# Performance work log

Hardware: AMD Instinct MI355X
Metric: run time of the kernel (lower is better)

The kernel has to match this reference:

```python
import jax, jax.numpy as jnp
import numpy as np

B, R, S, P = 32768, 16, 128, 128  # particles, rotations, num_sphs, num_projections


def setup_inputs() -> dict:
    key = jax.random.key(0)
    k1, k2, k3 = jax.random.split(key, 3)
    weight_scale = np.sqrt(6.0 / (S + P))  # RandomUniform(-scale, scale) init
    x_real = jax.random.normal(k1, (B, R, S), dtype=jnp.float32)
    x_imag = jax.random.normal(k2, (B, R, S), dtype=jnp.float32)
    projection = jax.random.uniform(k3, (R, S, P), dtype=jnp.float32,
                                    minval=-weight_scale, maxval=weight_scale)
    return {"x_real": x_real, "x_imag": x_imag, "projection": projection}


def reference(x_real, x_imag, projection):
    # complex input (B, R, S); real weight (R, S, P) cast to complex64
    x = jax.lax.complex(x_real, x_imag)
    w = projection.astype(x.dtype)
    # contraction over num_sphs (fused GEMM instead of expand_dims*mul+sum)
    sph_projected = jnp.einsum('brs,rsp->brp', x, w)  # (B, R, P) complex64
    # conversion == 'abs'
    return jnp.abs(sph_projected)
```

## Files before the change

### kernel.cpp

```cpp
#include <hip/hip_runtime.h>
#include <hip/hip_bf16.h>
#include <math.h>


typedef __attribute__((ext_vector_type(8))) __bf16 bf16x8;
typedef __attribute__((ext_vector_type(4))) float f32x4;

#define R_TOT 16
#define S_TOT 128
#define P_TOT 128
#define RS 2048
#define RP 2048
#define ROWS_PER_BLOCK 256
#define STRIP 16
#define NSTRIPS (ROWS_PER_BLOCK / STRIP)

typedef const __attribute__((address_space(1))) void* gas_t;
typedef __attribute__((address_space(3))) void* las_t;

__global__ __launch_bounds__(256, 3) void cproj_kernel(
    const float* __restrict__ x_real,
    const float* __restrict__ x_imag,
    const float* __restrict__ proj,
    float* __restrict__ out)
{
    __shared__ __attribute__((aligned(16))) float xb[2][2][STRIP][128];

    const int tid  = threadIdx.x;
    const int r    = blockIdx.x & 15;
    const int br   = blockIdx.x >> 4;
    const int lane = tid & 63;
    const int wid  = tid >> 6;
    const int m    = lane & 15;
    const int g    = lane >> 4;
    const int b_base = br * ROWS_PER_BLOCK;

    const int st_arr = wid >> 1;
    const int st_r0  = (wid & 1) * 8;
    const float* xsrc = (st_arr == 0) ? x_real : x_imag;

#define STAGE(bufi, strip_)                                                    \
    do {                                                                       \
        _Pragma("unroll")                                                      \
        for (int i = 0; i < 4; ++i) {                                          \
            const int row = st_r0 + 2 * i + (lane >> 5);                       \
            const int gb  = b_base + (strip_) * STRIP + row;                   \
            const float* gp = xsrc + (size_t)gb * RS + r * S_TOT               \
                              + (((lane & 31) ^ (row & 7)) << 2);              \
            __builtin_amdgcn_global_load_lds(                                  \
                (gas_t)gp, (las_t)&xb[bufi][st_arr][st_r0 + 2 * i][0],         \
                16, 0, 0);                                                     \
        }                                                                      \
    } while (0)

    STAGE(0, 0);

    bf16x8 wf[2][4];
    {
        const float* wrp = proj + (size_t)r * (S_TOT * P_TOT) + wid * 32 + m;
        #pragma unroll
        for (int nt = 0; nt < 2; ++nt) {
            #pragma unroll
            for (int kk = 0; kk < 4; ++kk) {
                bf16x8 w;
                #pragma unroll
                for (int j = 0; j < 8; ++j) {
                    w[j] = (__bf16)wrp[(size_t)(kk * 32 + g * 8 + j) * P_TOT
                                       + nt * 16];
                }
                wf[nt][kk] = w;
            }
        }
    }
    __syncthreads();

    for (int s = 0; s < NSTRIPS; ++s) {
        const int buf = s & 1;
        if (s + 1 < NSTRIPS) STAGE(buf ^ 1, s + 1);
        __builtin_amdgcn_sched_barrier(0);

        bf16x8 ar[2][4];
        #pragma unroll
        for (int a = 0; a < 2; ++a) {
            #pragma unroll
            for (int kk = 0; kk < 4; ++kk) {
                const int c0 = kk * 8 + 2 * g;
                const int s0 = (c0 ^ (m & 7)) << 2;
                const int s1 = ((c0 + 1) ^ (m & 7)) << 2;
                f32x4 lo = *(const f32x4*)&xb[buf][a][m][s0];
                f32x4 hi = *(const f32x4*)&xb[buf][a][m][s1];
                bf16x8 t;
                #pragma unroll
                for (int j = 0; j < 4; ++j) {
                    t[j]     = (__bf16)lo[j];
                    t[j + 4] = (__bf16)hi[j];
                }
                ar[a][kk] = t;
            }
        }

        f32x4 acc[2][2];
        #pragma unroll
        for (int nt = 0; nt < 2; ++nt) {
            acc[nt][0] = (f32x4)0.0f;
            acc[nt][1] = (f32x4)0.0f;
        }
        #pragma unroll
        for (int kk = 0; kk < 4; ++kk) {
            #pragma unroll
            for (int nt = 0; nt < 2; ++nt) {
                acc[nt][0] = __builtin_amdgcn_mfma_f32_16x16x32_bf16(
                    ar[0][kk], wf[nt][kk], acc[nt][0], 0, 0, 0);
                acc[nt][1] = __builtin_amdgcn_mfma_f32_16x16x32_bf16(
                    ar[1][kk], wf[nt][kk], acc[nt][1], 0, 0, 0);
            }
        }

        float ov[2][4];
        #pragma unroll
        for (int nt = 0; nt < 2; ++nt) {
            #pragma unroll
            for (int j = 0; j < 4; ++j) {
                float re = acc[nt][0][j];
                float im = acc[nt][1][j];
                ov[nt][j] = sqrtf(re * re + im * im);
            }
        }

        if (s + 1 < NSTRIPS) __syncthreads();

        float* po = out + (size_t)(b_base + s * STRIP + g * 4) * RP
                    + r * P_TOT + wid * 32 + m;
        #pragma unroll
        for (int nt = 0; nt < 2; ++nt) {
            #pragma unroll
            for (int j = 0; j < 4; ++j) {
                po[(size_t)j * RP + nt * 16] = ov[nt][j];
            }
        }
    }
#undef STAGE
}

extern "C" void kernel_launch(void* const* d_in, const int* in_sizes, int n_in,
                              void* d_out, int out_size, void* d_ws, size_t ws_size,
                              hipStream_t stream) {
    const float* x_real = (const float*)d_in[0];
    const float* x_imag = (const float*)d_in[1];
    const float* proj   = (const float*)d_in[2];
    float* out = (float*)d_out;

    dim3 grid(R_TOT * 128);
    dim3 block(256);
    cproj_kernel<<<grid, block, 0, stream>>>(x_real, x_imag, proj, out);
}
```

Before: 155.8 us.

## Triple-buffer strip staging with explicit vmcnt waits and fully unrolled loop

Replaces the double-buffered LDS staging with a three-deep ring that prefetches two strips ahead. Each strip is guarded by an explicit s_waitcnt vmcnt count plus a raw s_barrier instead of __syncthreads, and the strip loop is unrolled by hand so those counts can be literal constants. The intent is to keep more global loads in flight and let output stores stay outstanding instead of draining at each barrier. This uses more LDS, which may cut occupancy, and correctness depends on the hand-counted vmcnt values matching the real numbers of loads and stores in flight.

```diff
diff --git a/kernel.cpp b/kernel.cpp
--- a/kernel.cpp
+++ b/kernel.cpp
@@ -13,7 +13,7 @@
 #define RP 2048
 #define ROWS_PER_BLOCK 256
 #define STRIP 16
-#define NSTRIPS (ROWS_PER_BLOCK / STRIP)
+#define NSTRIPS 16
 
 typedef const __attribute__((address_space(1))) void* gas_t;
 typedef __attribute__((address_space(3))) void* las_t;
@@ -24,7 +24,7 @@
     const float* __restrict__ proj,
     float* __restrict__ out)
 {
-    __shared__ __attribute__((aligned(16))) float xb[2][2][STRIP][128];
+    __shared__ __attribute__((aligned(16))) float xb[3][2][STRIP][128];
 
     const int tid  = threadIdx.x;
     const int r    = blockIdx.x & 15;
@@ -39,21 +39,20 @@
     const int st_r0  = (wid & 1) * 8;
     const float* xsrc = (st_arr == 0) ? x_real : x_imag;
 
-#define STAGE(bufi, strip_)                                                    \
-    do {                                                                       \
-        _Pragma("unroll")                                                      \
-        for (int i = 0; i < 4; ++i) {                                          \
-            const int row = st_r0 + 2 * i + (lane >> 5);                       \
-            const int gb  = b_base + (strip_) * STRIP + row;                   \
-            const float* gp = xsrc + (size_t)gb * RS + r * S_TOT               \
-                              + (((lane & 31) ^ (row & 7)) << 2);              \
-            __builtin_amdgcn_global_load_lds(                                  \
-                (gas_t)gp, (las_t)&xb[bufi][st_arr][st_r0 + 2 * i][0],         \
-                16, 0, 0);                                                     \
-        }                                                                      \
+#define STAGE(strip_)                                                         \
+    do {                                                                      \
+        _Pragma("unroll")                                                     \
+        for (int i = 0; i < 4; ++i) {                                         \
+            const int row = st_r0 + 2 * i + (lane >> 5);                      \
+            const int gb  = b_base + (strip_) * STRIP + row;                  \
+            const float* gp = xsrc + (size_t)gb * RS + r * S_TOT              \
+                              + (((lane & 31) ^ (row & 7)) << 2);             \
+            __builtin_amdgcn_global_load_lds(                                 \
+                (gas_t)gp,                                                    \
+                (las_t)&xb[(strip_) % 3][st_arr][st_r0 + 2 * i][0],           \
+                16, 0, 0);                                                    \
+        }                                                                     \
     } while (0)
-
-    STAGE(0, 0);
 
     bf16x8 wf[2][4];
     {
@@ -72,73 +71,79 @@
             }
         }
     }
-    __syncthreads();
+    asm volatile("s_waitcnt vmcnt(0)" ::: "memory");
 
-    for (int s = 0; s < NSTRIPS; ++s) {
-        const int buf = s & 1;
-        if (s + 1 < NSTRIPS) STAGE(buf ^ 1, s + 1);
-        __builtin_amdgcn_sched_barrier(0);
+    STAGE(0);
+    STAGE(1);
 
-        bf16x8 ar[2][4];
-        #pragma unroll
-        for (int a = 0; a < 2; ++a) {
-            #pragma unroll
-            for (int kk = 0; kk < 4; ++kk) {
-                const int c0 = kk * 8 + 2 * g;
-                const int s0 = (c0 ^ (m & 7)) << 2;
-                const int s1 = ((c0 + 1) ^ (m & 7)) << 2;
-                f32x4 lo = *(const f32x4*)&xb[buf][a][m][s0];
-                f32x4 hi = *(const f32x4*)&xb[buf][a][m][s1];
-                bf16x8 t;
-                #pragma unroll
-                for (int j = 0; j < 4; ++j) {
-                    t[j]     = (__bf16)lo[j];
-                    t[j + 4] = (__bf16)hi[j];
-                }
-                ar[a][kk] = t;
-            }
-        }
+#define ITER(s_, vm_)                                                         \
+    {                                                                         \
+        asm volatile("s_waitcnt vmcnt(" #vm_ ")" ::: "memory");               \
+        __builtin_amdgcn_s_barrier();                                         \
+        __builtin_amdgcn_sched_barrier(0);                                    \
+        if ((s_) + 2 < NSTRIPS) STAGE((s_) + 2);                              \
+        bf16x8 ar[2][4];                                                      \
+        _Pragma("unroll")                                                     \
+        for (int a = 0; a < 2; ++a) {                                         \
+            _Pragma("unroll")                                                 \
+            for (int kk = 0; kk < 4; ++kk) {                                  \
+                const int c0  = kk * 8 + 2 * g;                               \
+                const int s0i = ((c0) ^ (m & 7)) << 2;                        \
+                const int s1i = ((c0 + 1) ^ (m & 7)) << 2;                    \
+                f32x4 lo = *(const f32x4*)&xb[(s_) % 3][a][m][s0i];           \
+                f32x4 hi = *(const f32x4*)&xb[(s_) % 3][a][m][s1i];           \
+                bf16x8 t;                                                     \
+                _Pragma("unroll")                                             \
+                for (int j = 0; j < 4; ++j) {                                 \
+                    t[j]     = (__bf16)lo[j];                                 \
+                    t[j + 4] = (__bf16)hi[j];                                 \
+                }                                                             \
+                ar[a][kk] = t;                                                \
+            }                                                                 \
+        }                                                                     \
+        f32x4 acc[2][2];                                     \
+        acc[0][0] = (f32x4)0.0f; acc[0][1] = (f32x4)0.0f;                     \
+        acc[1][0] = (f32x4)0.0f; acc[1][1] = (f32x4)0.0f;                     \
+        _Pragma("unroll")                                                     \
+        for (int kk = 0; kk < 4; ++kk) {                                      \
+            _Pragma("unroll")                                                 \
+            for (int nt = 0; nt < 2; ++nt) {                                  \
+                acc[nt][0] = __builtin_amdgcn_mfma_f32_16x16x32_bf16(         \
+                    ar[0][kk], wf[nt][kk], acc[nt][0], 0, 0, 0);              \
+                acc[nt][1] = __builtin_amdgcn_mfma_f32_16x16x32_bf16(         \
+                    ar[1][kk], wf[nt][kk], acc[nt][1], 0, 0, 0);              \
+            }                                                                 \
+        }                                                                     \
+        float* po = out + (size_t)(b_base + (s_) * STRIP + g * 4) * RP        \
+                    + r * P_TOT + wid * 32 + m;                               \
+        _Pragma("unroll")                                                     \
+        for (int nt = 0; nt < 2; ++nt) {                                      \
+            _Pragma("unroll")                                                 \
+            for (int j = 0; j < 4; ++j) {                                     \
+                float re = acc[nt][0][j];                                     \
+                float im = acc[nt][1][j];                                     \
+                po[(size_t)j * RP + nt * 16] = sqrtf(re * re + im * im);      \
+            }                                                                 \
+        }                                                                     \
+    }
 
-        f32x4 acc[2][2];
-        #pragma unroll
-        for (int nt = 0; nt < 2; ++nt) {
-            acc[nt][0] = (f32x4)0.0f;
-            acc[nt][1] = (f32x4)0.0f;
-        }
-        #pragma unroll
-        for (int kk = 0; kk < 4; ++kk) {
-            #pragma unroll
-            for (int nt = 0; nt < 2; ++nt) {
-                acc[nt][0] = __builtin_amdgcn_mfma_f32_16x16x32_bf16(
-                    ar[0][kk], wf[nt][kk], acc[nt][0], 0, 0, 0);
-                acc[nt][1] = __builtin_amdgcn_mfma_f32_16x16x32_bf16(
-                    ar[1][kk], wf[nt][kk], acc[nt][1], 0, 0, 0);
-            }
-        }
-
-        float ov[2][4];
-        #pragma unroll
-        for (int nt = 0; nt < 2; ++nt) {
-            #pragma unroll
-            for (int j = 0; j < 4; ++j) {
-                float re = acc[nt][0][j];
-                float im = acc[nt][1][j];
-                ov[nt][j] = sqrtf(re * re + im * im);
-            }
-        }
-
-        if (s + 1 < NSTRIPS) __syncthreads();
-
-        float* po = out + (size_t)(b_base + s * STRIP + g * 4) * RP
-                    + r * P_TOT + wid * 32 + m;
-        #pragma unroll
-        for (int nt = 0; nt < 2; ++nt) {
-            #pragma unroll
-            for (int j = 0; j < 4; ++j) {
-                po[(size_t)j * RP + nt * 16] = ov[nt][j];
-            }
-        }
-    }
+    ITER(0, 4)
+    ITER(1, 12)
+    ITER(2, 20)
+    ITER(3, 20)
+    ITER(4, 20)
+    ITER(5, 20)
+    ITER(6, 20)
+    ITER(7, 20)
+    ITER(8, 20)
+    ITER(9, 20)
+    ITER(10, 20)
+    ITER(11, 20)
+    ITER(12, 20)
+    ITER(13, 20)
+    ITER(14, 20)
+    ITER(15, 16)
+#undef ITER
 #undef STAGE
 }
 
```

After: 164.3 us. +5.4%, slower.
